# Performance work log

Measured on AMD Instinct MI355X. Metric: run time of the kernel, lower is better.

The kernel has to match this reference:

```python
import jax, jax.numpy as jnp
import numpy as np

N, F, B, D = 16384, 256, 48, 8


def setup_inputs() -> dict:
    key = jax.random.key(0)
    k_x, k_e, k_w, k_b = jax.random.split(key, 4)
    x = jax.random.normal(k_x, (N, F), dtype=jnp.float32)
    # per-feature sorted bin boundaries -> left edges and positive widths
    boundaries = jnp.sort(jax.random.uniform(k_e, (F, B + 1), dtype=jnp.float32,
                                             minval=-3.0, maxval=3.0), axis=-1)
    edges = boundaries[:, :-1]                     # [F, B]
    width = jnp.diff(boundaries, axis=-1)          # [F, B], > 0
    bound = 1.0 / np.sqrt(B)                       # nn.Linear default init
    W = jax.random.uniform(k_w, (F, B, D), dtype=jnp.float32, minval=-bound, maxval=bound)
    b = jax.random.uniform(k_b, (F, D), dtype=jnp.float32, minval=-bound, maxval=bound)
    return {"x": x, "edges": edges, "width": width, "W": W, "b": b}


def reference(x, edges, width, W, b):
    # piecewise-linear encoding: [N, F, B]
    h = (x[:, :, None] - edges) / width
    h = jnp.concatenate([
        jnp.minimum(h[..., :1], 1.0),          # first bin: clamp_max(1)
        jnp.clip(h[..., 1:-1], 0.0, 1.0),      # middle bins: clamp(0, 1)
        jnp.maximum(h[..., -1:], 0.0),         # last bin: clamp_min(0)
    ], axis=-1)
    # per-feature tiny Linear(B -> D), then concat over features
    out = jnp.einsum('nfb,fbd->nfd', h, W) + b   # [N, F, D]
    return out.reshape(x.shape[0], -1)           # [N, F*D]
```

## Files before the change

### kernel.cpp

```cpp
#include <hip/hip_runtime.h>


#define NN 16384
#define FF 256
#define BB 48
#define DD 8

#define FT 16
#define NSPLIT 64
#define NPB (NN / NSPLIT)

#define ESTR 17
#define CSTR (49 * DD + 4)

__global__ __launch_bounds__(256, 4)
void cple_kernel(const float* __restrict__ X,
                 const float* __restrict__ Edg,
                 const float* __restrict__ Wid,
                 const float* __restrict__ W,
                 const float* __restrict__ Bias,
                 float* __restrict__ Out)
{
    __shared__ float sE[49 * ESTR];
    __shared__ float sR[48 * ESTR];
    __shared__ float sC[FT * CSTR];

    const int tid = threadIdx.x;
    const int f0  = blockIdx.x * FT;
    const int ns  = blockIdx.y;

    {
        const float4* Wt4 = (const float4*)(W + (size_t)f0 * BB * DD);
        for (int idx4 = tid; idx4 < FT * BB * DD / 4; idx4 += 256) {
            float4 v = Wt4[idx4];
            int idx = idx4 * 4;
            int f   = idx / (BB * DD);
            int rem = idx - f * (BB * DD);
            int b   = rem >> 3;
            int d   = rem & 7;
            float* dst = &sC[f * CSTR + (b + 1) * DD + d];
            dst[0] = v.x; dst[1] = v.y; dst[2] = v.z; dst[3] = v.w;
        }
    }
    for (int idx = tid; idx < FT * BB; idx += 256) {
        int f = idx / BB;
        int j = idx - f * BB;
        sE[j * ESTR + f] = Edg[(size_t)(f0 + f) * BB + j];
        sR[j * ESTR + f] = 1.0f / Wid[(size_t)(f0 + f) * BB + j];
    }
    if (tid < FT) sE[48 * ESTR + tid] = __builtin_inff();
    __syncthreads();

    if (tid < FT * DD) {
        int f = tid >> 3;
        int d = tid & 7;
        float acc = Bias[(size_t)(f0 + f) * DD + d];
        float* c = &sC[f * CSTR + d];
        c[0] = acc;
        #pragma unroll
        for (int b = 1; b <= BB; ++b) {
            acc += c[b * DD];
            c[b * DD] = acc;
        }
    }
    __syncthreads();

    const int slot = tid & 31;
    const int f_l  = slot >> 1;
    const int half = slot & 1;
    const int r    = tid >> 5;

    const float* cF = &sC[f_l * CSTR + half * 4];
    const int fcol  = f0 + f_l;
    const float* xp = X + fcol;
    float* op = Out + (size_t)f0 * DD + slot * 4;

    const int n0 = ns * NPB + r;
    #pragma unroll 4
    for (int i = 0; i < NPB / 8; ++i) {
        int n = n0 + i * 8;
        float x = xp[(size_t)n * FF];

        int k = 0;
        #pragma unroll
        for (int w = 32; w >= 1; w >>= 1)
            k += (x >= sE[(k + w) * ESTR + f_l]) ? w : 0;
        float t = (x - sE[k * ESTR + f_l]) * sR[k * ESTR + f_l];

        float4 lo = *(const float4*)(cF + k * DD);
        float4 hi = *(const float4*)(cF + k * DD + DD);
        float4 o;
        o.x = fmaf(t, hi.x - lo.x, lo.x);
        o.y = fmaf(t, hi.y - lo.y, lo.y);
        o.z = fmaf(t, hi.z - lo.z, lo.z);
        o.w = fmaf(t, hi.w - lo.w, lo.w);

        *(float4*)(op + (size_t)n * (FF * DD)) = o;
    }
}

extern "C" void kernel_launch(void* const* d_in, const int* in_sizes, int n_in,
                              void* d_out, int out_size, void* d_ws, size_t ws_size,
                              hipStream_t stream) {
    const float* x     = (const float*)d_in[0];
    const float* edges = (const float*)d_in[1];
    const float* width = (const float*)d_in[2];
    const float* W     = (const float*)d_in[3];
    const float* b     = (const float*)d_in[4];
    float* out = (float*)d_out;

    dim3 grid(FF / FT, NSPLIT);
    cple_kernel<<<grid, 256, 0, stream>>>(x, edges, width, W, b, out);
}
```

Baseline: 193.7 us.

## Restructure bin search with register coarse thresholds and per-thread full-row output

Changes the thread mapping so each thread handles a whole feature row of 8 outputs instead of half a row, writing two float4 per sample. Shared-memory layouts move from bin-major to feature-major, so edges load as float4 and the W copy becomes contiguous. The six-step binary search over shared memory is replaced by five register-cached coarse comparisons plus one 8-wide linear scan using two float4 loads. This is meant to cut shared-memory traffic and dependent LDS latency per sample, but it may introduce LDS bank conflicts because stride-52 and stride-396 rows are read with data-dependent offsets, and it doubles the number of float4 loads each thread issues.

Measured after the change: 220.4 us. 13.8% more time.

```diff
diff --git a/kernel.cpp b/kernel.cpp
--- a/kernel.cpp
+++ b/kernel.cpp
@@ -10,8 +10,9 @@
 #define NSPLIT 64
 #define NPB (NN / NSPLIT)
 
-#define ESTR 17
-#define CSTR (49 * DD + 4)
+#define ESTR 52
+#define RSTR 48
+#define CSTR 396
 
 __global__ __launch_bounds__(256, 4)
 void cple_kernel(const float* __restrict__ X,
@@ -21,14 +22,24 @@
                  const float* __restrict__ Bias,
                  float* __restrict__ Out)
 {
-    __shared__ float sE[49 * ESTR];
-    __shared__ float sR[48 * ESTR];
-    __shared__ float sC[FT * CSTR];
+    __shared__ float sEv[FT * ESTR];
+    __shared__ float sR [FT * RSTR];
+    __shared__ float sC [FT * CSTR];
 
     const int tid = threadIdx.x;
     const int f0  = blockIdx.x * FT;
     const int ns  = blockIdx.y;
 
+    if (tid < FT * BB / 4) {
+        const float4* E4 = (const float4*)(Edg + (size_t)f0 * BB);
+        float4 v = E4[tid];
+        int f = tid / 12, j4 = tid % 12;
+        *(float4*)&sEv[f * ESTR + j4 * 4] = v;
+    }
+    for (int idx = tid; idx < FT * BB; idx += 256) {
+        int f = idx / BB, j = idx - f * BB;
+        sR[f * RSTR + j] = 1.0f / Wid[(size_t)f0 * BB + idx];
+    }
     {
         const float4* Wt4 = (const float4*)(W + (size_t)f0 * BB * DD);
         for (int idx4 = tid; idx4 < FT * BB * DD / 4; idx4 += 256) {
@@ -36,24 +47,14 @@
             int idx = idx4 * 4;
             int f   = idx / (BB * DD);
             int rem = idx - f * (BB * DD);
-            int b   = rem >> 3;
-            int d   = rem & 7;
-            float* dst = &sC[f * CSTR + (b + 1) * DD + d];
+            float* dst = &sC[f * CSTR + DD + rem];
             dst[0] = v.x; dst[1] = v.y; dst[2] = v.z; dst[3] = v.w;
         }
     }
-    for (int idx = tid; idx < FT * BB; idx += 256) {
-        int f = idx / BB;
-        int j = idx - f * BB;
-        sE[j * ESTR + f] = Edg[(size_t)(f0 + f) * BB + j];
-        sR[j * ESTR + f] = 1.0f / Wid[(size_t)(f0 + f) * BB + j];
-    }
-    if (tid < FT) sE[48 * ESTR + tid] = __builtin_inff();
     __syncthreads();
 
     if (tid < FT * DD) {
-        int f = tid >> 3;
-        int d = tid & 7;
+        int f = tid >> 3, d = tid & 7;
         float acc = Bias[(size_t)(f0 + f) * DD + d];
         float* c = &sC[f * CSTR + d];
         c[0] = acc;
@@ -65,37 +66,55 @@
     }
     __syncthreads();
 
-    const int slot = tid & 31;
-    const int f_l  = slot >> 1;
-    const int half = slot & 1;
-    const int r    = tid >> 5;
+    const int f_l = tid & 15;
+    const int n_l = tid >> 4;
+    const float* eF = &sEv[f_l * ESTR];
+    const float* rF = &sR [f_l * RSTR];
+    const float* cF = &sC [f_l * CSTR];
+    const float* xp = X + (f0 + f_l);
+    float* op = Out + (size_t)(f0 + f_l) * DD;
 
-    const float* cF = &sC[f_l * CSTR + half * 4];
-    const int fcol  = f0 + f_l;
-    const float* xp = X + fcol;
-    float* op = Out + (size_t)f0 * DD + slot * 4;
+    const float c8  = eF[8],  c16 = eF[16], c24 = eF[24];
+    const float c32 = eF[32], c40 = eF[40];
 
-    const int n0 = ns * NPB + r;
+    const int n0 = ns * NPB + n_l;
     #pragma unroll 4
-    for (int i = 0; i < NPB / 8; ++i) {
-        int n = n0 + i * 8;
+    for (int i = 0; i < NPB / 16; ++i) {
+        int n = n0 + i * 16;
         float x = xp[(size_t)n * FF];
 
         int k = 0;
-        #pragma unroll
-        for (int w = 32; w >= 1; w >>= 1)
-            k += (x >= sE[(k + w) * ESTR + f_l]) ? w : 0;
-        float t = (x - sE[k * ESTR + f_l]) * sR[k * ESTR + f_l];
+        k += (x >= c8)  ? 8 : 0;
+        k += (x >= c16) ? 8 : 0;
+        k += (x >= c24) ? 8 : 0;
+        k += (x >= c32) ? 8 : 0;
+        k += (x >= c40) ? 8 : 0;
 
-        float4 lo = *(const float4*)(cF + k * DD);
-        float4 hi = *(const float4*)(cF + k * DD + DD);
-        float4 o;
-        o.x = fmaf(t, hi.x - lo.x, lo.x);
-        o.y = fmaf(t, hi.y - lo.y, lo.y);
-        o.z = fmaf(t, hi.z - lo.z, lo.z);
-        o.w = fmaf(t, hi.w - lo.w, lo.w);
+        float4 fa = *(const float4*)(eF + k);
+        float4 fb = *(const float4*)(eF + k + 4);
+        k += (x >= fa.y) + (x >= fa.z) + (x >= fa.w)
+           + (x >= fb.x) + (x >= fb.y) + (x >= fb.z) + (x >= fb.w);
 
-        *(float4*)(op + (size_t)n * (FF * DD)) = o;
+        float t = (x - eF[k]) * rF[k];
+        const float* cK = cF + k * DD;
+        float4 l0 = *(const float4*)(cK);
+        float4 l1 = *(const float4*)(cK + 4);
+        float4 h0 = *(const float4*)(cK + 8);
+        float4 h1 = *(const float4*)(cK + 12);
+
+        float4 o0, o1;
+        o0.x = fmaf(t, h0.x - l0.x, l0.x);
+        o0.y = fmaf(t, h0.y - l0.y, l0.y);
+        o0.z = fmaf(t, h0.z - l0.z, l0.z);
+        o0.w = fmaf(t, h0.w - l0.w, l0.w);
+        o1.x = fmaf(t, h1.x - l1.x, l1.x);
+        o1.y = fmaf(t, h1.y - l1.y, l1.y);
+        o1.z = fmaf(t, h1.z - l1.z, l1.z);
+        o1.w = fmaf(t, h1.w - l1.w, l1.w);
+
+        float4* o = (float4*)(op + (size_t)n * (FF * DD));
+        o[0] = o0;
+        o[1] = o1;
     }
 }
 
```
